# Kernel optimization log

Measured on AMD Instinct MI355X. Metric: run time of the kernel, lower is better.

## Reference

```python
import jax, jax.numpy as jnp
import numpy as np

B, T, F = 2048, 60, 89
H = 1024
OUT = 30  # output_predicted_chords


def setup_inputs() -> dict:
    key = jax.random.key(0)
    k1, k2, k3, k4 = jax.random.split(key, 4)
    # small init scale keeps the relu-activated recurrence numerically stable
    s = 0.02
    return {
        "x": jax.random.normal(k1, (B, T, F), dtype=jnp.float32),
        "W": jax.random.normal(k2, (F, 4 * H), dtype=jnp.float32) * s,
        "U": jax.random.normal(k3, (H, 4 * H), dtype=jnp.float32) * s,
        "b": jnp.zeros((4 * H,), dtype=jnp.float32),
        "Wd": jax.random.normal(k4, (H, OUT), dtype=jnp.float32) * s,
        "bd": jnp.zeros((OUT,), dtype=jnp.float32),
    }


def _lstm_last_h(x, W, U, b):
    """Keras LSTM(activation='relu', recurrent_activation='sigmoid').
    Gate order in Keras kernels: i, f, c (candidate), o.
    Returns last hidden state h_T of shape [B, H]."""
    Bsz = x.shape[0]
    Hdim = U.shape[0]
    # precompute input projections for all timesteps: [T, B, 4H]
    xz = jnp.einsum('btf,fg->tbg', x, W) + b

    def step(carry, xz_t):
        h, c = carry
        z = xz_t + h @ U                      # [B, 4H]
        i, f, g, o = jnp.split(z, 4, axis=-1)
        i = jax.nn.sigmoid(i)
        f = jax.nn.sigmoid(f)
        g = jax.nn.relu(g)                    # activation='relu' on candidate
        o = jax.nn.sigmoid(o)
        c = f * c + i * g
        h = o * jax.nn.relu(c)                # activation='relu' on cell output
        return (h, c), None

    h0 = jnp.zeros((Bsz, Hdim), dtype=x.dtype)
    c0 = jnp.zeros((Bsz, Hdim), dtype=x.dtype)
    (hT, _), _ = jax.lax.scan(step, (h0, c0), xz)
    return hT


def reference(x, W, U, b, Wd, bd):
    # LSTM(return_sequences=True) then take x[:, -1, :] == last hidden state
    hT = _lstm_last_h(x, W, U, b)             # [B, H]
    y = hT @ Wd + bd                           # [B, OUT]
    return y.reshape(-1, OUT, 1)               # [B, 30, 1]
```

## Files before the change

kernel.cpp:

```cpp
#include <hip/hip_runtime.h>
#include <cstdint>
#include <cstddef>

#define Bsz 2048
#define Tseq 60
#define Fin 89
#define Hd 1024
#define G4 4096
#define KXP 128
#define NOUT 30

typedef _Float16 half8 __attribute__((ext_vector_type(8)));
typedef float f32x4 __attribute__((ext_vector_type(4)));

__device__ __forceinline__ void gload_lds16(const void* g, void* l) {
  __builtin_amdgcn_global_load_lds((const __attribute__((address_space(1))) void*)g,
                                   (__attribute__((address_space(3))) void*)l,
                                   16, 0, 0);
}

__device__ __forceinline__ float sigmoidf_fast(float x) {
  return 1.0f / (1.0f + __expf(-x));
}


__global__ __launch_bounds__(256) void convert_x(const float* __restrict__ x,
                                                 _Float16* __restrict__ xp) {
  int idx = blockIdx.x * 256 + threadIdx.x;
  int k = idx % KXP;
  int b = (idx / KXP) % Bsz;
  int t = idx / (KXP * Bsz);
  float v = (k < Fin) ? x[((size_t)b * Tseq + t) * Fin + k] : 0.0f;
  xp[idx] = (_Float16)v;
}

__global__ __launch_bounds__(256) void transpose_W(const float* __restrict__ W,
                                                   _Float16* __restrict__ Wpt) {
  __shared__ float tile[32][33];
  int n0 = blockIdx.x * 32;
  int k0 = blockIdx.y * 32;
  int tx = threadIdx.x, ty = threadIdx.y;
  for (int i = ty; i < 32; i += 8) {
    int k = k0 + i;
    tile[i][tx] = (k < Fin) ? W[(size_t)k * G4 + n0 + tx] : 0.0f;
  }
  __syncthreads();
  for (int i = ty; i < 32; i += 8)
    Wpt[(size_t)(n0 + i) * KXP + k0 + tx] = (_Float16)tile[tx][i];
}

__global__ __launch_bounds__(256) void transpose_U(const float* __restrict__ U,
                                                   _Float16* __restrict__ Upt) {
  __shared__ float tile[32][33];
  int n0 = blockIdx.x * 32;
  int k0 = blockIdx.y * 32;
  int tx = threadIdx.x, ty = threadIdx.y;
  for (int i = ty; i < 32; i += 8)
    tile[i][tx] = U[(size_t)(k0 + i) * G4 + n0 + tx];
  __syncthreads();
  for (int i = ty; i < 32; i += 8)
    Upt[(size_t)(n0 + i) * Hd + k0 + tx] = (_Float16)tile[tx][i];
}

__global__ __launch_bounds__(512, 1) void lstm_step(
    const _Float16* __restrict__ xp_t,
    const _Float16* __restrict__ Wpt,
    const _Float16* __restrict__ Upt,
    const float*    __restrict__ bias,
    const _Float16* __restrict__ h_in,
    _Float16*       __restrict__ h_out,
    float*          __restrict__ cst,
    int skip_h)
{
  __shared__ __align__(16) _Float16 As[3 * 8192];
  __shared__ __align__(16) _Float16 Bs[3 * 16384];

  const int tid  = threadIdx.x;
  const int wave = tid >> 6;
  const int lane = tid & 63;
  const int quad = lane >> 4;
  const int l16  = lane & 15;

  const int id  = blockIdx.x;
  const int xcd = id & 7, loc = id >> 3;
  const int jpanel = 4 * (xcd & 3) + (loc & 3);
  const int mpanel = 8 * (xcd >> 2) + (loc >> 2);
  const int m0 = mpanel * 128;
  const int j0 = jpanel * 64;

  const int srow = lane >> 2;
  const int qg   = (lane & 3) ^ ((lane >> 3) & 3);
  const int sA   = quad ^ ((l16 >> 1) & 3);

  const int mhalf = wave >> 2;
  const int nq    = wave & 3;
  const int j  = j0 + 16 * nq + l16;
  const int aoff = l16 * 32 + sA * 8;

  float bv[4];
#pragma unroll
  for (int p = 0; p < 4; ++p) bv[p] = bias[p * Hd + j];

  f32x4 acc[4][4];
#pragma unroll
  for (int mi = 0; mi < 4; ++mi)
#pragma unroll
    for (int p = 0; p < 4; ++p)
      acc[mi][p] = f32x4{bv[p], bv[p], bv[p], bv[p]};

  auto stage = [&](int buf, int r) {
    const _Float16* Ab; const _Float16* Bb; int strA, strB, k0;
    if (r < 2) { Ab = xp_t; strA = KXP; Bb = Wpt; strB = KXP; k0 = r * 64; }
    else       { Ab = h_in; strA = Hd;  Bb = Upt; strB = Hd;  k0 = (r - 2) * 64; }
    _Float16* Ad = &As[buf * 8192];
    _Float16* Bd = &Bs[buf * 16384];
#pragma unroll
    for (int ii = 0; ii < 2; ++ii) {
      int i = ii * 8 + wave;
      int st = i >> 3, ci = i & 7;
      gload_lds16(Ab + (size_t)(m0 + ci * 16 + srow) * strA + k0 + st * 32 + qg * 8,
                  Ad + st * 4096 + ci * 512);
    }
#pragma unroll
    for (int ii = 0; ii < 4; ++ii) {
      int i = ii * 8 + wave;
      int st = i >> 4, ci = i & 15;
      int gn = (ci >> 2) * Hd + j0 + 16 * (ci & 3) + srow;
      gload_lds16(Bb + (size_t)gn * strB + k0 + st * 32 + qg * 8,
                  Bd + st * 8192 + ci * 512);
    }
  };

  auto compute = [&](int buf) {
    const __attribute__((address_space(3))) _Float16* As3 =
        (const __attribute__((address_space(3))) _Float16*)&As[buf * 8192];
    const __attribute__((address_space(3))) _Float16* Bs3 =
        (const __attribute__((address_space(3))) _Float16*)&Bs[buf * 16384];
    half8 a0[4], b0[4], a1[4], b1[4];
#pragma unroll
    for (int mi = 0; mi < 4; ++mi)
      asm volatile("ds_read_b128 %0, %1" : "=v"(a0[mi])
                   : "v"(As3 + (4 * mhalf + mi) * 512 + aoff) : "memory");
#pragma unroll
    for (int p = 0; p < 4; ++p)
      asm volatile("ds_read_b128 %0, %1" : "=v"(b0[p])
                   : "v"(Bs3 + (4 * p + nq) * 512 + aoff) : "memory");
#pragma unroll
    for (int mi = 0; mi < 4; ++mi)
      asm volatile("ds_read_b128 %0, %1" : "=v"(a1[mi])
                   : "v"(As3 + 4096 + (4 * mhalf + mi) * 512 + aoff) : "memory");
#pragma unroll
    for (int p = 0; p < 4; ++p)
      asm volatile("ds_read_b128 %0, %1" : "=v"(b1[p])
                   : "v"(Bs3 + 8192 + (4 * p + nq) * 512 + aoff) : "memory");
    asm volatile("s_waitcnt lgkmcnt(8)" ::: "memory");
    __builtin_amdgcn_sched_barrier(0);
#pragma unroll
    for (int mi = 0; mi < 4; ++mi)
#pragma unroll
      for (int p = 0; p < 4; ++p)
        acc[mi][p] = __builtin_amdgcn_mfma_f32_16x16x32_f16(a0[mi], b0[p],
                                                            acc[mi][p], 0, 0, 0);
    asm volatile("s_waitcnt lgkmcnt(0)" ::: "memory");
    __builtin_amdgcn_sched_barrier(0);
#pragma unroll
    for (int mi = 0; mi < 4; ++mi)
#pragma unroll
      for (int p = 0; p < 4; ++p)
        acc[mi][p] = __builtin_amdgcn_mfma_f32_16x16x32_f16(a1[mi], b1[p],
                                                            acc[mi][p], 0, 0, 0);
  };

  const int NR = skip_h ? 2 : 18;

  stage(0, 0);
  stage(1, 1);
  if (NR > 2) stage(2, 2);

  for (int r = 0; r < NR; ++r) {
    const int cur = r % 3;
    if (NR - r >= 3)      asm volatile("s_waitcnt vmcnt(12)" ::: "memory");
    else if (NR - r == 2) asm volatile("s_waitcnt vmcnt(6)"  ::: "memory");
    else                  asm volatile("s_waitcnt vmcnt(0)"  ::: "memory");
    __builtin_amdgcn_sched_barrier(0);
    __builtin_amdgcn_s_barrier();
    __builtin_amdgcn_s_setprio(1);
    compute(cur);
    __builtin_amdgcn_s_setprio(0);
    __builtin_amdgcn_s_barrier();
    if (r + 3 < NR) stage(cur, r + 3);
  }

#pragma unroll
  for (int mi = 0; mi < 4; ++mi) {
#pragma unroll
    for (int rr = 0; rr < 4; ++rr) {
      int row = m0 + 64 * mhalf + mi * 16 + quad * 4 + rr;
      size_t idx = (size_t)row * Hd + j;
      float iv = sigmoidf_fast(acc[mi][0][rr]);
      float fv = sigmoidf_fast(acc[mi][1][rr]);
      float gv = fmaxf(acc[mi][2][rr], 0.0f);
      float ov = sigmoidf_fast(acc[mi][3][rr]);
      float cprev = skip_h ? 0.0f : cst[idx];
      float cv = fv * cprev + iv * gv;
      cst[idx] = cv;
      float hv = ov * fmaxf(cv, 0.0f);
      h_out[idx] = (_Float16)hv;
    }
  }
}

__global__ __launch_bounds__(256) void final_dense(const _Float16* __restrict__ h,
                                                   const float* __restrict__ Wd,
                                                   const float* __restrict__ bd,
                                                   float* __restrict__ y) {
  __shared__ float hs[Hd];
  __shared__ float red[8][32];
  int bi = blockIdx.x;
  for (int k = threadIdx.x; k < Hd; k += 256)
    hs[k] = (float)h[(size_t)bi * Hd + k];
  __syncthreads();
  int o  = threadIdx.x & 31;
  int ch = threadIdx.x >> 5;
  float p = 0.0f;
  if (o < NOUT) {
    int k0 = ch * (Hd / 8);
    for (int k = k0; k < k0 + (Hd / 8); ++k)
      p += hs[k] * Wd[(size_t)k * NOUT + o];
  }
  red[ch][o] = p;
  __syncthreads();
  if (threadIdx.x < NOUT) {
    float s = bd[threadIdx.x];
    for (int c2 = 0; c2 < 8; ++c2) s += red[c2][threadIdx.x];
    y[(size_t)bi * NOUT + threadIdx.x] = s;
  }
}


extern "C" void kernel_launch(void* const* d_in, const int* in_sizes, int n_in,
                              void* d_out, int out_size, void* d_ws, size_t ws_size,
                              hipStream_t stream) {
  const float* x  = (const float*)d_in[0];
  const float* W  = (const float*)d_in[1];
  const float* U  = (const float*)d_in[2];
  const float* b  = (const float*)d_in[3];
  const float* Wd = (const float*)d_in[4];
  const float* bd = (const float*)d_in[5];
  float* y = (float*)d_out;

  char* ws = (char*)d_ws;
  _Float16* xp  = (_Float16*)ws; ws += (size_t)Tseq * Bsz * KXP * 2;
  _Float16* Wpt = (_Float16*)ws; ws += (size_t)G4 * KXP * 2;
  _Float16* Upt = (_Float16*)ws; ws += (size_t)G4 * Hd * 2;
  _Float16* hb0 = (_Float16*)ws; ws += (size_t)Bsz * Hd * 2;
  _Float16* hb1 = (_Float16*)ws; ws += (size_t)Bsz * Hd * 2;
  float*    cst = (float*)ws;    ws += (size_t)Bsz * Hd * 4;

  convert_x<<<(Tseq * Bsz * KXP) / 256, 256, 0, stream>>>(x, xp);
  transpose_W<<<dim3(G4 / 32, KXP / 32), dim3(32, 8), 0, stream>>>(W, Wpt);
  transpose_U<<<dim3(G4 / 32, Hd / 32), dim3(32, 8), 0, stream>>>(U, Upt);

  for (int t = 0; t < Tseq; ++t) {
    const _Float16* hin  = ((t - 1) & 1) ? hb1 : hb0;
    _Float16*       hout = (t & 1) ? hb1 : hb0;
    lstm_step<<<dim3((Bsz / 128) * (G4 / 256)), 512, 0, stream>>>(
        xp + (size_t)t * (Bsz * KXP), Wpt, Upt, b,
        (t == 0) ? hb0 : hin, hout, cst, (t == 0) ? 1 : 0);
  }

  final_dense<<<Bsz, 256, 0, stream>>>(hb1, Wd, bd, y);
}
```

Before: 1.865 ms.

## Split LSTM step GEMM pipeline into six 32-wide K sub-stages with deeper prefetch

Each 64-wide K stage of the triple-buffered LDS pipeline is split into two 32-wide sub-stages held in six slots, with loads issued four sub-stages ahead. The next global-to-LDS load is now issued inside each phase, right after that phase's LDS reads and before its MFMAs, with vmcnt waits sized per phase. The aim is to overlap global loads with compute more evenly and shorten waits on memory at each step. In exchange the K loop has twice as many iterations, so there are twice as many workgroup barriers and shorter MFMA bursts between them.

After: 1.788 ms. 1.04x faster.

```diff
diff --git a/kernel.cpp b/kernel.cpp
--- a/kernel.cpp
+++ b/kernel.cpp
@@ -21,6 +21,15 @@
 
 __device__ __forceinline__ float sigmoidf_fast(float x) {
   return 1.0f / (1.0f + __expf(-x));
+}
+
+__device__ __forceinline__ void vmwait(int n) {
+  switch (n) {
+    case 9:  asm volatile("s_waitcnt vmcnt(9)" ::: "memory"); break;
+    case 6:  asm volatile("s_waitcnt vmcnt(6)" ::: "memory"); break;
+    case 3:  asm volatile("s_waitcnt vmcnt(3)" ::: "memory"); break;
+    default: asm volatile("s_waitcnt vmcnt(0)" ::: "memory"); break;
+  }
 }
 
 
@@ -72,8 +81,8 @@
     float*          __restrict__ cst,
     int skip_h)
 {
-  __shared__ __align__(16) _Float16 As[3 * 8192];
-  __shared__ __align__(16) _Float16 Bs[3 * 16384];
+  __shared__ __align__(16) _Float16 As[6 * 4096];
+  __shared__ __align__(16) _Float16 Bs[6 * 8192];
 
   const int tid  = threadIdx.x;
   const int wave = tid >> 6;
@@ -108,87 +117,70 @@
     for (int p = 0; p < 4; ++p)
       acc[mi][p] = f32x4{bv[p], bv[p], bv[p], bv[p]};
 
-  auto stage = [&](int buf, int r) {
+  const int S = skip_h ? 4 : 36;
+
+  auto stageSub = [&](int s) {
     const _Float16* Ab; const _Float16* Bb; int strA, strB, k0;
-    if (r < 2) { Ab = xp_t; strA = KXP; Bb = Wpt; strB = KXP; k0 = r * 64; }
-    else       { Ab = h_in; strA = Hd;  Bb = Upt; strB = Hd;  k0 = (r - 2) * 64; }
-    _Float16* Ad = &As[buf * 8192];
-    _Float16* Bd = &Bs[buf * 16384];
+    if (s < 4) { Ab = xp_t; strA = KXP; Bb = Wpt; strB = KXP; k0 = s * 32; }
+    else       { Ab = h_in; strA = Hd;  Bb = Upt; strB = Hd;  k0 = (s - 4) * 32; }
+    int h = s % 6;
+    _Float16* Ad = &As[h * 4096];
+    _Float16* Bd = &Bs[h * 8192];
+    gload_lds16(Ab + (size_t)(m0 + wave * 16 + srow) * strA + k0 + qg * 8,
+                Ad + wave * 512);
 #pragma unroll
     for (int ii = 0; ii < 2; ++ii) {
-      int i = ii * 8 + wave;
-      int st = i >> 3, ci = i & 7;
-      gload_lds16(Ab + (size_t)(m0 + ci * 16 + srow) * strA + k0 + st * 32 + qg * 8,
-                  Ad + st * 4096 + ci * 512);
-    }
-#pragma unroll
-    for (int ii = 0; ii < 4; ++ii) {
-      int i = ii * 8 + wave;
-      int st = i >> 4, ci = i & 15;
+      int ci = ii * 8 + wave;
       int gn = (ci >> 2) * Hd + j0 + 16 * (ci & 3) + srow;
-      gload_lds16(Bb + (size_t)gn * strB + k0 + st * 32 + qg * 8,
-                  Bd + st * 8192 + ci * 512);
+      gload_lds16(Bb + (size_t)gn * strB + k0 + qg * 8, Bd + ci * 512);
     }
   };
 
-  auto compute = [&](int buf) {
+  auto phase = [&](int s, int vmN) {
+    int h = s % 6;
     const __attribute__((address_space(3))) _Float16* As3 =
-        (const __attribute__((address_space(3))) _Float16*)&As[buf * 8192];
+        (const __attribute__((address_space(3))) _Float16*)&As[h * 4096];
     const __attribute__((address_space(3))) _Float16* Bs3 =
-        (const __attribute__((address_space(3))) _Float16*)&Bs[buf * 16384];
-    half8 a0[4], b0[4], a1[4], b1[4];
+        (const __attribute__((address_space(3))) _Float16*)&Bs[h * 8192];
+    half8 a[4], b[4];
 #pragma unroll
     for (int mi = 0; mi < 4; ++mi)
-      asm volatile("ds_read_b128 %0, %1" : "=v"(a0[mi])
+      asm volatile("ds_read_b128 %0, %1" : "=v"(a[mi])
                    : "v"(As3 + (4 * mhalf + mi) * 512 + aoff) : "memory");
 #pragma unroll
     for (int p = 0; p < 4; ++p)
-      asm volatile("ds_read_b128 %0, %1" : "=v"(b0[p])
+      asm volatile("ds_read_b128 %0, %1" : "=v"(b[p])
                    : "v"(Bs3 + (4 * p + nq) * 512 + aoff) : "memory");
-#pragma unroll
-    for (int mi = 0; mi < 4; ++mi)
-      asm volatile("ds_read_b128 %0, %1" : "=v"(a1[mi])
-                   : "v"(As3 + 4096 + (4 * mhalf + mi) * 512 + aoff) : "memory");
-#pragma unroll
-    for (int p = 0; p < 4; ++p)
-      asm volatile("ds_read_b128 %0, %1" : "=v"(b1[p])
-                   : "v"(Bs3 + 8192 + (4 * p + nq) * 512 + aoff) : "memory");
-    asm volatile("s_waitcnt lgkmcnt(8)" ::: "memory");
+    if (s + 4 < S) stageSub(s + 4);
+    vmwait(vmN);
     __builtin_amdgcn_sched_barrier(0);
-#pragma unroll
-    for (int mi = 0; mi < 4; ++mi)
-#pragma unroll
-      for (int p = 0; p < 4; ++p)
-        acc[mi][p] = __builtin_amdgcn_mfma_f32_16x16x32_f16(a0[mi], b0[p],
-                                                            acc[mi][p], 0, 0, 0);
+    __builtin_amdgcn_s_barrier();
     asm volatile("s_waitcnt lgkmcnt(0)" ::: "memory");
     __builtin_amdgcn_sched_barrier(0);
+    __builtin_amdgcn_s_setprio(1);
 #pragma unroll
     for (int mi = 0; mi < 4; ++mi)
 #pragma unroll
       for (int p = 0; p < 4; ++p)
-        acc[mi][p] = __builtin_amdgcn_mfma_f32_16x16x32_f16(a1[mi], b1[p],
+        acc[mi][p] = __builtin_amdgcn_mfma_f32_16x16x32_f16(a[mi], b[p],
                                                             acc[mi][p], 0, 0, 0);
-  };
-
-  const int NR = skip_h ? 2 : 18;
-
-  stage(0, 0);
-  stage(1, 1);
-  if (NR > 2) stage(2, 2);
-
-  for (int r = 0; r < NR; ++r) {
-    const int cur = r % 3;
-    if (NR - r >= 3)      asm volatile("s_waitcnt vmcnt(12)" ::: "memory");
-    else if (NR - r == 2) asm volatile("s_waitcnt vmcnt(6)"  ::: "memory");
-    else                  asm volatile("s_waitcnt vmcnt(0)"  ::: "memory");
-    __builtin_amdgcn_sched_barrier(0);
-    __builtin_amdgcn_s_barrier();
-    __builtin_amdgcn_s_setprio(1);
-    compute(cur);
     __builtin_amdgcn_s_setprio(0);
     __builtin_amdgcn_s_barrier();
-    if (r + 3 < NR) stage(cur, r + 3);
+  };
+
+  stageSub(0);
+  stageSub(1);
+  stageSub(2);
+  stageSub(3);
+  vmwait(9);
+  __builtin_amdgcn_sched_barrier(0);
+  __builtin_amdgcn_s_barrier();
+
+  int s = 0;
+  for (; s < S - 4; ++s) phase(s, 9);
+  for (; s < S; ++s) {
+    int rem = S - 2 - s;
+    phase(s, rem >= 3 ? 9 : (rem > 0 ? 3 * rem : 0));
   }
 
 #pragma unroll
```
